# Kernel optimization log

Measured on AMD Instinct MI355X. Metric: run time of the kernel, lower is better.

Reference implementation:

```python
import jax, jax.numpy as jnp
import numpy as np

N = 100000      # nodes
E = 1600000     # edges (avg degree 16)
D_IN, H, D_OUT = 128, 64, 40


def setup_inputs() -> dict:
    key = jax.random.key(0)
    k = jax.random.split(key, 6)
    x = jax.random.normal(k[0], (N, D_IN), dtype=jnp.float32)
    edge_index = jax.random.randint(k[1], (2, E), 0, N, dtype=jnp.int32)
    W1 = jax.random.normal(k[2], (D_IN, H), dtype=jnp.float32) / np.sqrt(D_IN)
    b1 = jnp.zeros((H,), dtype=jnp.float32)
    W2 = jax.random.normal(k[3], (H, D_OUT), dtype=jnp.float32) / np.sqrt(H)
    b2 = jnp.zeros((D_OUT,), dtype=jnp.float32)
    return {"x": x, "edge_index": edge_index, "W1": W1, "b1": b1, "W2": W2, "b2": b2}


def _gcn_conv(h, src, dst, dinv, W, b):
    # PyG GCNConv: linear transform, then D^-1/2 (A+I) D^-1/2 aggregation, then bias.
    h = h @ W                                   # [N, F]
    w = dinv[src] * dinv[dst]                   # [E] symmetric norm edge weights
    msg = h[src] * w[:, None]                   # [E, F] gather + scale
    agg = jax.ops.segment_sum(msg, dst, num_segments=N)  # scatter-add to dst
    agg = agg + h * (dinv * dinv)[:, None]      # self-loop contribution deg^-1 * h
    return agg + b


def reference(x, edge_index, W1, b1, W2, b2):
    src, dst = edge_index[0], edge_index[1]
    # degree with self-loops (in-degree at dst, source_to_target flow)
    deg = 1.0 + jax.ops.segment_sum(jnp.ones((E,), dtype=x.dtype), dst, num_segments=N)
    dinv = jax.lax.rsqrt(deg)
    # dropout (p=0.6) is identity in eval mode
    h = jax.nn.relu(_gcn_conv(x, src, dst, dinv, W1, b1))
    out = _gcn_conv(h, src, dst, dinv, W2, b2)
    return jax.nn.log_softmax(out, axis=1)
```

## Files before the change

### kernel.cpp

```cpp
#include <hip/hip_runtime.h>
#include <math.h>

#define D_IN  128
#define H_DIM 64
#define D_OUT 40
#define BW_SHIFT 9
#define BW_NODES 512
#define BINA_CHUNK 8192
#define BUCKET_CAP 9216

typedef unsigned int uint32;

__device__ __forceinline__ unsigned short f2bf(float v) {
    uint32 b = __float_as_uint(v);
    b += 0x7fffu + ((b >> 16) & 1u);
    return (unsigned short)(b >> 16);
}
__device__ __forceinline__ float bf2f(unsigned short u) {
    return __uint_as_float(((uint32)u) << 16);
}
__device__ __forceinline__ void acc8(float* a, uint4 v) {
    a[0] += __uint_as_float(v.x << 16);
    a[1] += __uint_as_float(v.x & 0xffff0000u);
    a[2] += __uint_as_float(v.y << 16);
    a[3] += __uint_as_float(v.y & 0xffff0000u);
    a[4] += __uint_as_float(v.z << 16);
    a[5] += __uint_as_float(v.z & 0xffff0000u);
    a[6] += __uint_as_float(v.w << 16);
    a[7] += __uint_as_float(v.w & 0xffff0000u);
}
__device__ __forceinline__ void unpack8(float* a, uint4 v) {
    a[0] = __uint_as_float(v.x << 16);
    a[1] = __uint_as_float(v.x & 0xffff0000u);
    a[2] = __uint_as_float(v.y << 16);
    a[3] = __uint_as_float(v.y & 0xffff0000u);
    a[4] = __uint_as_float(v.z << 16);
    a[5] = __uint_as_float(v.z & 0xffff0000u);
    a[6] = __uint_as_float(v.w << 16);
    a[7] = __uint_as_float(v.w & 0xffff0000u);
}

__global__ void cursor_init_kernel(int* __restrict__ gcursor, int NBUCK) {
    int i = blockIdx.x * 256 + threadIdx.x;
    if (i < NBUCK) gcursor[i] = i * BUCKET_CAP;
}

__global__ __launch_bounds__(256) void binA_scatter_kernel(const int* __restrict__ src,
                                                           const int* __restrict__ dst,
                                                           int* __restrict__ gcursor,
                                                           uint32* __restrict__ binned,
                                                           int E, int NBUCK) {
    __shared__ int cnt[1024];
    __shared__ int lbase[1024];
    int t = threadIdx.x;
    for (int i = t; i < NBUCK; i += 256) cnt[i] = 0;
    __syncthreads();
    int e0 = blockIdx.x * BINA_CHUNK;
    int e1 = min(e0 + BINA_CHUNK, E);
    for (int e = e0 + t; e < e1; e += 256)
        atomicAdd(&cnt[dst[e] >> BW_SHIFT], 1);
    __syncthreads();
    for (int i = t; i < NBUCK; i += 256) {
        int c = cnt[i];
        lbase[i] = c ? atomicAdd(&gcursor[i], c) : 0;
        cnt[i] = 0;
    }
    __syncthreads();
    for (int e = e0 + t; e < e1; e += 256) {
        int d = dst[e];
        int bk = d >> BW_SHIFT;
        int p = lbase[bk] + atomicAdd(&cnt[bk], 1);
        binned[p] = (((uint32)(d & (BW_NODES - 1))) << 23) | (uint32)src[e];
    }
}

__global__ __launch_bounds__(256) void phaseB_kernel(uint32* __restrict__ binned,
                                                     const int* __restrict__ gcur_end,
                                                     int* __restrict__ rows,
                                                     float* __restrict__ dinv,
                                                     int N) {
    __shared__ uint32 sedge[BUCKET_CAP];
    __shared__ int deg[BW_NODES];
    __shared__ int sa[BW_NODES], sb[BW_NODES];
    __shared__ int cur[BW_NODES];
    int b = blockIdx.x;
    int node0 = b << BW_SHIFT;
    int nn = min(BW_NODES, N - node0);
    int base = b * BUCKET_CAP;
    int cnt = gcur_end[b] - base;
    int t = threadIdx.x;
    deg[t] = 0; deg[t + 256] = 0;
    __syncthreads();
    for (int e = t; e < cnt; e += 256) {
        uint32 v = binned[base + e];
        sedge[e] = v;
        atomicAdd(&deg[v >> 23], 1);
    }
    __syncthreads();
    for (int i = t; i < nn; i += 256)
        dinv[node0 + i] = rsqrtf(1.0f + (float)deg[i]);
    sa[t] = deg[t]; sa[t + 256] = deg[t + 256];
    __syncthreads();
    int* pa = sa; int* pb = sb;
    for (int off = 1; off < BW_NODES; off <<= 1) {
        for (int i = t; i < BW_NODES; i += 256)
            pb[i] = pa[i] + ((i >= off) ? pa[i - off] : 0);
        __syncthreads();
        int* tmp = pa; pa = pb; pb = tmp;
    }
    for (int i = t; i < BW_NODES; i += 256)
        cur[i] = (i ? pa[i - 1] : 0);
    __syncthreads();
    int* rb = rows + b * 513;
    for (int i = t; i < nn; i += 256)
        rb[i] = base + cur[i];
    if (t == 0) rb[nn] = base + cnt;
    __syncthreads();
    for (int e = t; e < cnt; e += 256) {
        uint32 v = sedge[e];
        int doff = v >> 23;
        int p = base + atomicAdd(&cur[doff], 1);
        binned[p] = v & 0x7FFFFFu;
    }
}

__global__ __launch_bounds__(256) void gemm1_tn4(const float* __restrict__ x,
                                                 const float* __restrict__ W1,
                                                 const float* __restrict__ dinv,
                                                 unsigned short* __restrict__ h1s, int N) {
    __shared__ float sW[D_IN * H_DIM];
    int t = threadIdx.x;
    for (int i = t; i < D_IN * H_DIM / 4; i += 256)
        reinterpret_cast<float4*>(sW)[i] = reinterpret_cast<const float4*>(W1)[i];
    __syncthreads();

    int n = blockIdx.x * 64 + (t >> 2);
    if (n >= N) return;
    int c0 = (t & 3) * 16;
    const float4* xr = reinterpret_cast<const float4*>(x + (size_t)n * D_IN);

    float acc[16] = {};
    for (int k0 = 0; k0 < D_IN / 4; ++k0) {
        float4 xv = xr[k0];
        #pragma unroll
        for (int kk = 0; kk < 4; ++kk) {
            float xk = (kk == 0) ? xv.x : (kk == 1) ? xv.y : (kk == 2) ? xv.z : xv.w;
            const float* wrow = &sW[(4 * k0 + kk) * H_DIM + c0];
            #pragma unroll
            for (int c = 0; c < 4; ++c) {
                float4 wv = *reinterpret_cast<const float4*>(wrow + 4 * c);
                acc[4 * c + 0] += xk * wv.x;
                acc[4 * c + 1] += xk * wv.y;
                acc[4 * c + 2] += xk * wv.z;
                acc[4 * c + 3] += xk * wv.w;
            }
        }
    }
    float di = dinv[n];
    unsigned short* orow = h1s + (size_t)n * H_DIM + c0;
    #pragma unroll
    for (int c = 0; c < 4; ++c) {
        ushort4 u;
        u.x = f2bf(acc[4 * c + 0] * di);
        u.y = f2bf(acc[4 * c + 1] * di);
        u.z = f2bf(acc[4 * c + 2] * di);
        u.w = f2bf(acc[4 * c + 3] * di);
        *reinterpret_cast<ushort4*>(orow + 4 * c) = u;
    }
}

__global__ __launch_bounds__(256) void agg1_v4(const int* __restrict__ rows,
                                               const int* __restrict__ csr,
                                               const unsigned short* __restrict__ h1s,
                                               const float* __restrict__ dinv,
                                               const float* __restrict__ b1,
                                               float* __restrict__ z, int N) {
    int node = blockIdx.x * 4 + (threadIdx.x >> 6);
    if (node >= N) return;
    int lane = threadIdx.x & 63;
    int e  = lane >> 3;
    int fl = (lane & 7) * 8;
    int ridx = node + (node >> BW_SHIFT);
    int s0 = __builtin_amdgcn_readfirstlane(rows[ridx]);
    int s1 = __builtin_amdgcn_readfirstlane(rows[ridx + 1]);

    float a[8] = {};
    for (int base = s0; base < s1; base += 64) {
        int cnt = min(64, s1 - base);
        int myc = (lane < cnt) ? csr[base + lane] : 0;
        int j = 0;
        for (; j + 16 <= cnt; j += 16) {
            uint32 sa = (uint32)__shfl(myc, j + e);
            uint32 sb = (uint32)__shfl(myc, j + 8 + e);
            uint4 ha = *reinterpret_cast<const uint4*>(h1s + (size_t)(sa * H_DIM + fl));
            uint4 hb = *reinterpret_cast<const uint4*>(h1s + (size_t)(sb * H_DIM + fl));
            acc8(a, ha);
            acc8(a, hb);
        }
        for (; j < cnt; j += 8) {
            int idx = j + e;
            uint32 sa = (uint32)__shfl(myc, min(idx, cnt - 1));
            if (idx < cnt) {
                uint4 hv = *reinterpret_cast<const uint4*>(h1s + (size_t)(sa * H_DIM + fl));
                acc8(a, hv);
            }
        }
    }
    #pragma unroll
    for (int i = 0; i < 8; ++i) {
        a[i] += __shfl_xor(a[i], 8);
        a[i] += __shfl_xor(a[i], 16);
        a[i] += __shfl_xor(a[i], 32);
    }

    if (e == 0) {
        uint4 sv = *reinterpret_cast<const uint4*>(h1s + (size_t)node * H_DIM + fl);
        float sf[8];
        unpack8(sf, sv);
        float4 bv0 = *reinterpret_cast<const float4*>(b1 + fl);
        float4 bv1 = *reinterpret_cast<const float4*>(b1 + fl + 4);
        float di = dinv[node];
        float4 o0, o1;
        o0.x = fmaxf(0.f, di * (a[0] + sf[0]) + bv0.x);
        o0.y = fmaxf(0.f, di * (a[1] + sf[1]) + bv0.y);
        o0.z = fmaxf(0.f, di * (a[2] + sf[2]) + bv0.z);
        o0.w = fmaxf(0.f, di * (a[3] + sf[3]) + bv0.w);
        o1.x = fmaxf(0.f, di * (a[4] + sf[4]) + bv1.x);
        o1.y = fmaxf(0.f, di * (a[5] + sf[5]) + bv1.y);
        o1.z = fmaxf(0.f, di * (a[6] + sf[6]) + bv1.z);
        o1.w = fmaxf(0.f, di * (a[7] + sf[7]) + bv1.w);
        float* zr = z + (size_t)node * H_DIM + fl;
        *reinterpret_cast<float4*>(zr) = o0;
        *reinterpret_cast<float4*>(zr + 4) = o1;
    }
}

__global__ __launch_bounds__(256) void gemm2_tn2(const float* __restrict__ z,
                                                 const float* __restrict__ W2,
                                                 const float* __restrict__ dinv,
                                                 unsigned short* __restrict__ h2s, int N) {
    __shared__ float sW[H_DIM * D_OUT];
    int t = threadIdx.x;
    for (int i = t; i < H_DIM * D_OUT / 4; i += 256)
        reinterpret_cast<float4*>(sW)[i] = reinterpret_cast<const float4*>(W2)[i];
    __syncthreads();

    int n = blockIdx.x * 128 + (t >> 1);
    if (n >= N) return;
    int c0 = (t & 1) * 20;
    const float4* zr = reinterpret_cast<const float4*>(z + (size_t)n * H_DIM);

    float acc[20] = {};
    for (int k0 = 0; k0 < H_DIM / 4; ++k0) {
        float4 zv = zr[k0];
        #pragma unroll
        for (int kk = 0; kk < 4; ++kk) {
            float zk = (kk == 0) ? zv.x : (kk == 1) ? zv.y : (kk == 2) ? zv.z : zv.w;
            const float* wrow = &sW[(4 * k0 + kk) * D_OUT + c0];
            #pragma unroll
            for (int c = 0; c < 5; ++c) {
                float4 wv = *reinterpret_cast<const float4*>(wrow + 4 * c);
                acc[4 * c + 0] += zk * wv.x;
                acc[4 * c + 1] += zk * wv.y;
                acc[4 * c + 2] += zk * wv.z;
                acc[4 * c + 3] += zk * wv.w;
            }
        }
    }
    float di = dinv[n];
    unsigned short* orow = h2s + (size_t)n * D_OUT + c0;
    #pragma unroll
    for (int c = 0; c < 5; ++c) {
        ushort4 u;
        u.x = f2bf(acc[4 * c + 0] * di);
        u.y = f2bf(acc[4 * c + 1] * di);
        u.z = f2bf(acc[4 * c + 2] * di);
        u.w = f2bf(acc[4 * c + 3] * di);
        *reinterpret_cast<ushort4*>(orow + 4 * c) = u;
    }
}

__global__ __launch_bounds__(256) void agg2_v5(const int* __restrict__ rows,
                                               const int* __restrict__ csr,
                                               const unsigned short* __restrict__ h2s,
                                               const float* __restrict__ dinv,
                                               const float* __restrict__ b2,
                                               float* __restrict__ out, int N) {
    int node = blockIdx.x * 4 + (threadIdx.x >> 6);
    if (node >= N) return;
    int lane = threadIdx.x & 63;
    int g  = lane / 5;
    int r5 = lane - g * 5;
    int fl = r5 * 8;
    bool gact = g < 12;
    int ridx = node + (node >> BW_SHIFT);
    int s0 = __builtin_amdgcn_readfirstlane(rows[ridx]);
    int s1 = __builtin_amdgcn_readfirstlane(rows[ridx + 1]);

    float a[8] = {};
    for (int base = s0; base < s1; base += 64) {
        int cnt = min(64, s1 - base);
        int myc = (lane < cnt) ? csr[base + lane] : 0;
        for (int j = 0; j < cnt; j += 12) {
            int idx = j + g;
            uint32 sa = (uint32)__shfl(myc, min(idx, cnt - 1));
            if (gact && idx < cnt) {
                uint4 hv = *reinterpret_cast<const uint4*>(h2s + (size_t)(sa * D_OUT + fl));
                acc8(a, hv);
            }
        }
    }
    #pragma unroll
    for (int i = 0; i < 8; ++i)
        a[i] += __shfl(a[i], min(lane + 30, 63));
    #pragma unroll
    for (int i = 0; i < 8; ++i)
        a[i] += __shfl(a[i], min(lane + 15, 63));
    #pragma unroll
    for (int i = 0; i < 8; ++i)
        a[i] += __shfl(a[i], min(lane + 5, 63)) + __shfl(a[i], min(lane + 10, 63));

    bool act = lane < 5;
    float v[8];
    if (act) {
        uint4 sv = *reinterpret_cast<const uint4*>(h2s + (size_t)node * D_OUT + fl);
        float sf[8];
        unpack8(sf, sv);
        float4 bv0 = *reinterpret_cast<const float4*>(b2 + fl);
        float4 bv1 = *reinterpret_cast<const float4*>(b2 + fl + 4);
        float di = dinv[node];
        v[0] = di * (a[0] + sf[0]) + bv0.x;
        v[1] = di * (a[1] + sf[1]) + bv0.y;
        v[2] = di * (a[2] + sf[2]) + bv0.z;
        v[3] = di * (a[3] + sf[3]) + bv0.w;
        v[4] = di * (a[4] + sf[4]) + bv1.x;
        v[5] = di * (a[5] + sf[5]) + bv1.y;
        v[6] = di * (a[6] + sf[6]) + bv1.z;
        v[7] = di * (a[7] + sf[7]) + bv1.w;
    } else {
        #pragma unroll
        for (int i = 0; i < 8; ++i) v[i] = -INFINITY;
    }
    float lm = fmaxf(fmaxf(fmaxf(v[0], v[1]), fmaxf(v[2], v[3])),
                     fmaxf(fmaxf(v[4], v[5]), fmaxf(v[6], v[7])));
    float mm = lm;
    #pragma unroll
    for (int i = 0; i < 5; ++i) mm = fmaxf(mm, __shfl(lm, i));
    float le = 0.f;
    if (act) {
        #pragma unroll
        for (int i = 0; i < 8; ++i) le += __expf(v[i] - mm);
    }
    float es = 0.f;
    #pragma unroll
    for (int i = 0; i < 5; ++i) es += __shfl(le, i);
    float lse = __logf(es);
    if (act) {
        float4 o0 = make_float4(v[0] - mm - lse, v[1] - mm - lse, v[2] - mm - lse, v[3] - mm - lse);
        float4 o1 = make_float4(v[4] - mm - lse, v[5] - mm - lse, v[6] - mm - lse, v[7] - mm - lse);
        float* orow = out + (size_t)node * D_OUT + fl;
        *reinterpret_cast<float4*>(orow) = o0;
        *reinterpret_cast<float4*>(orow + 4) = o1;
    }
}

extern "C" void kernel_launch(void* const* d_in, const int* in_sizes, int n_in,
                              void* d_out, int out_size, void* d_ws, size_t ws_size,
                              hipStream_t stream) {
    const float* x  = (const float*)d_in[0];
    const int*   ei = (const int*)d_in[1];
    const float* W1 = (const float*)d_in[2];
    const float* b1 = (const float*)d_in[3];
    const float* W2 = (const float*)d_in[4];
    const float* b2 = (const float*)d_in[5];
    float* out = (float*)d_out;

    int N = in_sizes[0] / D_IN;
    int E = in_sizes[1] / 2;
    const int* src = ei;
    const int* dst = ei + E;
    int NBUCK = (N + BW_NODES - 1) / BW_NODES;

    char* p = (char*)d_ws;
    int*   gcursor = (int*)p;  p += 4096;
    int*   rows    = (int*)p;  p += ((size_t)NBUCK * 513 + 64) * 4;
    float* dinv    = (float*)p; p += (((size_t)N + 63) & ~(size_t)63) * 4;
    uint32* binned = (uint32*)p; p += (size_t)NBUCK * BUCKET_CAP * 4;
    unsigned short* h1s = (unsigned short*)p; p += (size_t)N * H_DIM * 2;
    float* z       = (float*)p; p += (size_t)N * H_DIM * 4;

    int binA_blocks = (E + BINA_CHUNK - 1) / BINA_CHUNK;

    cursor_init_kernel<<<(NBUCK + 255) / 256, 256, 0, stream>>>(gcursor, NBUCK);
    binA_scatter_kernel<<<binA_blocks, 256, 0, stream>>>(src, dst, gcursor, binned, E, NBUCK);
    phaseB_kernel<<<NBUCK, 256, 0, stream>>>(binned, gcursor, rows, dinv, N);
    int* csr = (int*)binned;

    gemm1_tn4<<<(N + 63) / 64, 256, 0, stream>>>(x, W1, dinv, h1s, N);
    agg1_v4<<<(N + 3) / 4, 256, 0, stream>>>(rows, csr, h1s, dinv, b1, z, N);

    unsigned short* h2s = h1s;
    gemm2_tn2<<<(N + 127) / 128, 256, 0, stream>>>(z, W2, dinv, h2s, N);
    agg2_v5<<<(N + 3) / 4, 256, 0, stream>>>(rows, csr, h2s, dinv, b2, out, N);
}
```

Before: 213.2 us.

## Process two destination nodes per wavefront in both aggregation kernels

Both gather/aggregate kernels now assign two destination nodes to each 64-lane wavefront and interleave their neighbor gathers, giving four independent 16-byte loads in flight per iteration. The aim is more memory-level parallelism and less per-node launch and reduction overhead. agg2 also moves from a 5x12 lane layout to an 8x8 layout with only 5 active feature lanes per group, which leaves 3 of 8 lanes idle. The cost is extra register pressure and wasted iterations when the two nodes have unequal degrees.

```diff
diff --git a/kernel.cpp b/kernel.cpp
--- a/kernel.cpp
+++ b/kernel.cpp
@@ -169,51 +169,66 @@
     }
 }
 
-__global__ __launch_bounds__(256) void agg1_v4(const int* __restrict__ rows,
+__global__ __launch_bounds__(256) void agg1_v5(const int* __restrict__ rows,
                                                const int* __restrict__ csr,
                                                const unsigned short* __restrict__ h1s,
                                                const float* __restrict__ dinv,
                                                const float* __restrict__ b1,
                                                float* __restrict__ z, int N) {
-    int node = blockIdx.x * 4 + (threadIdx.x >> 6);
-    if (node >= N) return;
+    int wid = threadIdx.x >> 6;
+    int nA = (blockIdx.x * 4 + wid) * 2;
+    if (nA >= N) return;
+    int nB = nA + 1;
+    bool hasB = nB < N;
     int lane = threadIdx.x & 63;
     int e  = lane >> 3;
     int fl = (lane & 7) * 8;
-    int ridx = node + (node >> BW_SHIFT);
-    int s0 = __builtin_amdgcn_readfirstlane(rows[ridx]);
-    int s1 = __builtin_amdgcn_readfirstlane(rows[ridx + 1]);
-
-    float a[8] = {};
-    for (int base = s0; base < s1; base += 64) {
-        int cnt = min(64, s1 - base);
-        int myc = (lane < cnt) ? csr[base + lane] : 0;
-        int j = 0;
-        for (; j + 16 <= cnt; j += 16) {
-            uint32 sa = (uint32)__shfl(myc, j + e);
-            uint32 sb = (uint32)__shfl(myc, j + 8 + e);
-            uint4 ha = *reinterpret_cast<const uint4*>(h1s + (size_t)(sa * H_DIM + fl));
-            uint4 hb = *reinterpret_cast<const uint4*>(h1s + (size_t)(sb * H_DIM + fl));
-            acc8(a, ha);
-            acc8(a, hb);
+    int ra = nA + (nA >> BW_SHIFT);
+    int s0A = __builtin_amdgcn_readfirstlane(rows[ra]);
+    int s1A = __builtin_amdgcn_readfirstlane(rows[ra + 1]);
+    int s0B = 0, s1B = 0;
+    if (hasB) {
+        int rb = nB + (nB >> BW_SHIFT);
+        s0B = __builtin_amdgcn_readfirstlane(rows[rb]);
+        s1B = __builtin_amdgcn_readfirstlane(rows[rb + 1]);
+    }
+
+    float aA[8] = {}, aB[8] = {};
+    const uint4 zero4 = make_uint4(0, 0, 0, 0);
+    int baseA = s0A, baseB = s0B;
+    while (baseA < s1A || baseB < s1B) {
+        int cA = (baseA < s1A) ? min(64, s1A - baseA) : 0;
+        int cB = (baseB < s1B) ? min(64, s1B - baseB) : 0;
+        int mycA = (lane < cA) ? csr[baseA + lane] : 0;
+        int mycB = (lane < cB) ? csr[baseB + lane] : 0;
+        int clA = max(cA - 1, 0), clB = max(cB - 1, 0);
+        int m = max(cA, cB);
+        for (int j = 0; j < m; j += 16) {
+            int i0 = j + e, i1 = j + 8 + e;
+            uint32 sA0 = (uint32)__shfl(mycA, min(i0, clA));
+            uint32 sA1 = (uint32)__shfl(mycA, min(i1, clA));
+            uint32 sB0 = (uint32)__shfl(mycB, min(i0, clB));
+            uint32 sB1 = (uint32)__shfl(mycB, min(i1, clB));
+            uint4 hA0 = (i0 < cA) ? *reinterpret_cast<const uint4*>(h1s + (size_t)(sA0 * H_DIM + fl)) : zero4;
+            uint4 hA1 = (i1 < cA) ? *reinterpret_cast<const uint4*>(h1s + (size_t)(sA1 * H_DIM + fl)) : zero4;
+            uint4 hB0 = (i0 < cB) ? *reinterpret_cast<const uint4*>(h1s + (size_t)(sB0 * H_DIM + fl)) : zero4;
+            uint4 hB1 = (i1 < cB) ? *reinterpret_cast<const uint4*>(h1s + (size_t)(sB1 * H_DIM + fl)) : zero4;
+            acc8(aA, hA0); acc8(aA, hA1);
+            acc8(aB, hB0); acc8(aB, hB1);
         }
-        for (; j < cnt; j += 8) {
-            int idx = j + e;
-            uint32 sa = (uint32)__shfl(myc, min(idx, cnt - 1));
-            if (idx < cnt) {
-                uint4 hv = *reinterpret_cast<const uint4*>(h1s + (size_t)(sa * H_DIM + fl));
-                acc8(a, hv);
-            }
-        }
+        baseA += cA; baseB += cB;
     }
     #pragma unroll
     for (int i = 0; i < 8; ++i) {
-        a[i] += __shfl_xor(a[i], 8);
-        a[i] += __shfl_xor(a[i], 16);
-        a[i] += __shfl_xor(a[i], 32);
-    }
-
-    if (e == 0) {
+        aA[i] += __shfl_xor(aA[i], 8);  aA[i] += __shfl_xor(aA[i], 16);  aA[i] += __shfl_xor(aA[i], 32);
+        aB[i] += __shfl_xor(aB[i], 8);  aB[i] += __shfl_xor(aB[i], 16);  aB[i] += __shfl_xor(aB[i], 32);
+    }
+    int sel = lane >> 3;
+    if (sel < 2 && (sel == 0 || hasB)) {
+        float av[8];
+        #pragma unroll
+        for (int i = 0; i < 8; ++i) av[i] = sel ? aB[i] : aA[i];
+        int node = nA + sel;
         uint4 sv = *reinterpret_cast<const uint4*>(h1s + (size_t)node * H_DIM + fl);
         float sf[8];
         unpack8(sf, sv);
@@ -221,14 +236,14 @@
         float4 bv1 = *reinterpret_cast<const float4*>(b1 + fl + 4);
         float di = dinv[node];
         float4 o0, o1;
-        o0.x = fmaxf(0.f, di * (a[0] + sf[0]) + bv0.x);
-        o0.y = fmaxf(0.f, di * (a[1] + sf[1]) + bv0.y);
-        o0.z = fmaxf(0.f, di * (a[2] + sf[2]) + bv0.z);
-        o0.w = fmaxf(0.f, di * (a[3] + sf[3]) + bv0.w);
-        o1.x = fmaxf(0.f, di * (a[4] + sf[4]) + bv1.x);
-        o1.y = fmaxf(0.f, di * (a[5] + sf[5]) + bv1.y);
-        o1.z = fmaxf(0.f, di * (a[6] + sf[6]) + bv1.z);
-        o1.w = fmaxf(0.f, di * (a[7] + sf[7]) + bv1.w);
+        o0.x = fmaxf(0.f, di * (av[0] + sf[0]) + bv0.x);
+        o0.y = fmaxf(0.f, di * (av[1] + sf[1]) + bv0.y);
+        o0.z = fmaxf(0.f, di * (av[2] + sf[2]) + bv0.z);
+        o0.w = fmaxf(0.f, di * (av[3] + sf[3]) + bv0.w);
+        o1.x = fmaxf(0.f, di * (av[4] + sf[4]) + bv1.x);
+        o1.y = fmaxf(0.f, di * (av[5] + sf[5]) + bv1.y);
+        o1.z = fmaxf(0.f, di * (av[6] + sf[6]) + bv1.z);
+        o1.w = fmaxf(0.f, di * (av[7] + sf[7]) + bv1.w);
         float* zr = z + (size_t)node * H_DIM + fl;
         *reinterpret_cast<float4*>(zr) = o0;
         *reinterpret_cast<float4*>(zr + 4) = o1;
@@ -280,82 +295,104 @@
     }
 }
 
-__global__ __launch_bounds__(256) void agg2_v5(const int* __restrict__ rows,
+__global__ __launch_bounds__(256) void agg2_v6(const int* __restrict__ rows,
                                                const int* __restrict__ csr,
                                                const unsigned short* __restrict__ h2s,
                                                const float* __restrict__ dinv,
                                                const float* __restrict__ b2,
                                                float* __restrict__ out, int N) {
-    int node = blockIdx.x * 4 + (threadIdx.x >> 6);
-    if (node >= N) return;
+    int wid = threadIdx.x >> 6;
+    int nA = (blockIdx.x * 4 + wid) * 2;
+    if (nA >= N) return;
+    int nB = nA + 1;
+    bool hasB = nB < N;
     int lane = threadIdx.x & 63;
-    int g  = lane / 5;
-    int r5 = lane - g * 5;
-    int fl = r5 * 8;
-    bool gact = g < 12;
-    int ridx = node + (node >> BW_SHIFT);
-    int s0 = __builtin_amdgcn_readfirstlane(rows[ridx]);
-    int s1 = __builtin_amdgcn_readfirstlane(rows[ridx + 1]);
-
-    float a[8] = {};
-    for (int base = s0; base < s1; base += 64) {
-        int cnt = min(64, s1 - base);
-        int myc = (lane < cnt) ? csr[base + lane] : 0;
-        for (int j = 0; j < cnt; j += 12) {
-            int idx = j + g;
-            uint32 sa = (uint32)__shfl(myc, min(idx, cnt - 1));
-            if (gact && idx < cnt) {
-                uint4 hv = *reinterpret_cast<const uint4*>(h2s + (size_t)(sa * D_OUT + fl));
-                acc8(a, hv);
-            }
+    int e  = lane >> 3;
+    int r  = lane & 7;
+    int fl = r * 8;
+    bool ract = r < 5;
+    int ra = nA + (nA >> BW_SHIFT);
+    int s0A = __builtin_amdgcn_readfirstlane(rows[ra]);
+    int s1A = __builtin_amdgcn_readfirstlane(rows[ra + 1]);
+    int s0B = 0, s1B = 0;
+    if (hasB) {
+        int rb = nB + (nB >> BW_SHIFT);
+        s0B = __builtin_amdgcn_readfirstlane(rows[rb]);
+        s1B = __builtin_amdgcn_readfirstlane(rows[rb + 1]);
+    }
+
+    float aA[8] = {}, aB[8] = {};
+    const uint4 zero4 = make_uint4(0, 0, 0, 0);
+    int baseA = s0A, baseB = s0B;
+    while (baseA < s1A || baseB < s1B) {
+        int cA = (baseA < s1A) ? min(64, s1A - baseA) : 0;
+        int cB = (baseB < s1B) ? min(64, s1B - baseB) : 0;
+        int mycA = (lane < cA) ? csr[baseA + lane] : 0;
+        int mycB = (lane < cB) ? csr[baseB + lane] : 0;
+        int clA = max(cA - 1, 0), clB = max(cB - 1, 0);
+        int m = max(cA, cB);
+        for (int j = 0; j < m; j += 16) {
+            int i0 = j + e, i1 = j + 8 + e;
+            uint32 sA0 = (uint32)__shfl(mycA, min(i0, clA));
+            uint32 sA1 = (uint32)__shfl(mycA, min(i1, clA));
+            uint32 sB0 = (uint32)__shfl(mycB, min(i0, clB));
+            uint32 sB1 = (uint32)__shfl(mycB, min(i1, clB));
+            uint4 hA0 = (ract && i0 < cA) ? *reinterpret_cast<const uint4*>(h2s + (size_t)(sA0 * D_OUT + fl)) : zero4;
+            uint4 hA1 = (ract && i1 < cA) ? *reinterpret_cast<const uint4*>(h2s + (size_t)(sA1 * D_OUT + fl)) : zero4;
+            uint4 hB0 = (ract && i0 < cB) ? *reinterpret_cast<const uint4*>(h2s + (size_t)(sB0 * D_OUT + fl)) : zero4;
+            uint4 hB1 = (ract && i1 < cB) ? *reinterpret_cast<const uint4*>(h2s + (size_t)(sB1 * D_OUT + fl)) : zero4;
+            acc8(aA, hA0); acc8(aA, hA1);
+            acc8(aB, hB0); acc8(aB, hB1);
         }
-    }
-    #pragma unroll
-    for (int i = 0; i < 8; ++i)
-        a[i] += __shfl(a[i], min(lane + 30, 63));
-    #pragma unroll
-    for (int i = 0; i < 8; ++i)
-        a[i] += __shfl(a[i], min(lane + 15, 63));
-    #pragma unroll
-    for (int i = 0; i < 8; ++i)
-        a[i] += __shfl(a[i], min(lane + 5, 63)) + __shfl(a[i], min(lane + 10, 63));
-
-    bool act = lane < 5;
+        baseA += cA; baseB += cB;
+    }
+    #pragma unroll
+    for (int i = 0; i < 8; ++i) {
+        aA[i] += __shfl_xor(aA[i], 8);  aA[i] += __shfl_xor(aA[i], 16);  aA[i] += __shfl_xor(aA[i], 32);
+        aB[i] += __shfl_xor(aB[i], 8);  aB[i] += __shfl_xor(aB[i], 16);  aB[i] += __shfl_xor(aB[i], 32);
+    }
+    int sel = lane >> 3;
+    bool actw = (sel < 2) && ract && (sel == 0 || hasB);
+    int node = nA + ((sel < 2) ? sel : 0);
     float v[8];
-    if (act) {
+    if (actw) {
+        float av[8];
+        #pragma unroll
+        for (int i = 0; i < 8; ++i) av[i] = sel ? aB[i] : aA[i];
         uint4 sv = *reinterpret_cast<const uint4*>(h2s + (size_t)node * D_OUT + fl);
         float sf[8];
         unpack8(sf, sv);
         float4 bv0 = *reinterpret_cast<const float4*>(b2 + fl);
         float4 bv1 = *reinterpret_cast<const float4*>(b2 + fl + 4);
         float di = dinv[node];
-        v[0] = di * (a[0] + sf[0]) + bv0.x;
-        v[1] = di * (a[1] + sf[1]) + bv0.y;
-        v[2] = di * (a[2] + sf[2]) + bv0.z;
-        v[3] = di * (a[3] + sf[3]) + bv0.w;
-        v[4] = di * (a[4] + sf[4]) + bv1.x;
-        v[5] = di * (a[5] + sf[5]) + bv1.y;
-        v[6] = di * (a[6] + sf[6]) + bv1.z;
-        v[7] = di * (a[7] + sf[7]) + bv1.w;
+        v[0] = di * (av[0] + sf[0]) + bv0.x;
+        v[1] = di * (av[1] + sf[1]) + bv0.y;
+        v[2] = di * (av[2] + sf[2]) + bv0.z;
+        v[3] = di * (av[3] + sf[3]) + bv0.w;
+        v[4] = di * (av[4] + sf[4]) + bv1.x;
+        v[5] = di * (av[5] + sf[5]) + bv1.y;
+        v[6] = di * (av[6] + sf[6]) + bv1.z;
+        v[7] = di * (av[7] + sf[7]) + bv1.w;
     } else {
         #pragma unroll
         for (int i = 0; i < 8; ++i) v[i] = -INFINITY;
     }
     float lm = fmaxf(fmaxf(fmaxf(v[0], v[1]), fmaxf(v[2], v[3])),
                      fmaxf(fmaxf(v[4], v[5]), fmaxf(v[6], v[7])));
-    float mm = lm;
-    #pragma unroll
-    for (int i = 0; i < 5; ++i) mm = fmaxf(mm, __shfl(lm, i));
+    int gb = (sel < 2) ? (sel << 3) : 0;
+    float mm = -INFINITY;
+    #pragma unroll
+    for (int i = 0; i < 5; ++i) mm = fmaxf(mm, __shfl(lm, gb + i));
     float le = 0.f;
-    if (act) {
+    if (actw) {
         #pragma unroll
         for (int i = 0; i < 8; ++i) le += __expf(v[i] - mm);
     }
     float es = 0.f;
     #pragma unroll
-    for (int i = 0; i < 5; ++i) es += __shfl(le, i);
+    for (int i = 0; i < 5; ++i) es += __shfl(le, gb + i);
     float lse = __logf(es);
-    if (act) {
+    if (actw) {
         float4 o0 = make_float4(v[0] - mm - lse, v[1] - mm - lse, v[2] - mm - lse, v[3] - mm - lse);
         float4 o1 = make_float4(v[4] - mm - lse, v[5] - mm - lse, v[6] - mm - lse, v[7] - mm - lse);
         float* orow = out + (size_t)node * D_OUT + fl;
@@ -397,9 +434,9 @@
     int* csr = (int*)binned;
 
     gemm1_tn4<<<(N + 63) / 64, 256, 0, stream>>>(x, W1, dinv, h1s, N);
-    agg1_v4<<<(N + 3) / 4, 256, 0, stream>>>(rows, csr, h1s, dinv, b1, z, N);
+    agg1_v5<<<(N + 7) / 8, 256, 0, stream>>>(rows, csr, h1s, dinv, b1, z, N);
 
     unsigned short* h2s = h1s;
     gemm2_tn2<<<(N + 127) / 128, 256, 0, stream>>>(z, W2, dinv, h2s, N);
-    agg2_v5<<<(N + 3) / 4, 256, 0, stream>>>(rows, csr, h2s, dinv, b2, out, N);
-}
+    agg2_v6<<<(N + 7) / 8, 256, 0, stream>>>(rows, csr, h2s, dinv, b2, out, N);
+}
```

Result: no change. 216.3 us (+1.5%).
